# Kernel optimization log

Hardware: AMD Instinct MI355X
Metric: run time of the kernel (lower is better)

## Reference

```python
import jax, jax.numpy as jnp
import numpy as np


def setup_inputs() -> dict:
    key = jax.random.key(0)
    k1, k2 = jax.random.split(key)
    hw, bs, c = 16384, 16, 256
    nq = 100
    return {
        "query_feat": jax.random.normal(k1, (hw, bs, c), dtype=jnp.float32),
        "support_feat": jax.random.normal(k2, (nq, bs, c), dtype=jnp.float32),
        "h": 128,
        "w": 128,
    }


def reference(query_feat, support_feat, h, w):
    # query_feat: [hw, bs, c], support_feat: [nq, bs, c]
    hw, bs, c = query_feat.shape
    nq = support_feat.shape[0]
    dtype = query_feat.dtype

    side_normalizer = jnp.array([w, h], dtype=dtype)[None, None, :]  # [1,1,2]

    q = jnp.transpose(query_feat, (1, 0, 2))    # [bs, hw, c]
    s = jnp.transpose(support_feat, (1, 0, 2))  # [bs, nq, c]

    # bmm(q, s^T) -> [bs, hw, nq]; transpose -> [bs, nq, hw]
    similarity_flat = jnp.einsum('bnc,bkc->bnk', s, q)        # [bs, nq, hw]
    similarity = similarity_flat.reshape(bs, nq, h, w)

    # coordinate grid: stack([grid_x, grid_y]) with 'ij' meshgrid, flattened to [hw, 2]
    ys = jnp.linspace(0.5, h - 0.5, h, dtype=jnp.float32)
    xs = jnp.linspace(0.5, w - 0.5, w, dtype=jnp.float32)
    grid_y, grid_x = jnp.meshgrid(ys, xs, indexing='ij')      # [h, w] each
    coord = jnp.stack([grid_x, grid_y], axis=-1).reshape(hw, 2)  # [hw, 2]

    similarity_softmax = jax.nn.softmax(similarity_flat, axis=-1)  # [bs, nq, hw]

    proposal_for_loss = jnp.einsum('bnk,kd->bnd', similarity_softmax, coord) / side_normalizer

    # peak masking: argmax -> one_hot -> reshape (w, h) [faithful to original swap] -> 3x3 max pool
    max_pos = jnp.argmax(similarity_flat, axis=-1)            # [bs, nq]
    max_mask = jax.nn.one_hot(max_pos, hw, dtype=jnp.float32).reshape(bs, nq, w, h)
    local_max_mask = jax.lax.reduce_window(
        max_mask, -jnp.inf, jax.lax.max,
        window_dimensions=(1, 1, 3, 3), window_strides=(1, 1, 1, 1),
        padding=((0, 0), (0, 0), (1, 1), (1, 1)),
    ).reshape(bs, nq, hw)                                     # [bs, nq, hw]

    local_sm = similarity_softmax * local_max_mask            # [bs, nq, hw]
    local_sm = local_sm / (jnp.sum(local_sm, axis=-1, keepdims=True) + 1e-10)
    proposals = jnp.einsum('bnk,kd->bnd', local_sm, coord) / side_normalizer

    return (proposal_for_loss, similarity, proposals)
```

## Files before the change

### kernel.cpp

```cpp
#include <hip/hip_runtime.h>
#include <math.h>

#define HW   16384
#define BS   16
#define C    256
#define NQ   100
#define NQP  112
#define Hh   128
#define Ww   128

#define SIM_OFF   3200
#define PROPS_OFF (3200 + 26214400)

#define BM 256
#define BK 32

typedef _Float16 half8 __attribute__((ext_vector_type(8)));
typedef float f32x4 __attribute__((ext_vector_type(4)));

__device__ __forceinline__ void gll16(const void* gp, void* lp) {
    __builtin_amdgcn_global_load_lds((const __attribute__((address_space(1))) void*)gp,
                                     (__attribute__((address_space(3))) void*)lp, 16, 0, 0);
}

__device__ __forceinline__ void split8(const float4 a, const float4 b, half8& hi, half8& lo) {
    float f[8] = {a.x, a.y, a.z, a.w, b.x, b.y, b.z, b.w};
    _Float16 h[8], l[8];
    #pragma unroll
    for (int i = 0; i < 8; ++i) {
        h[i] = (_Float16)f[i];
        l[i] = (_Float16)(f[i] - (float)h[i]);
    }
    hi = *(half8*)h;
    lo = *(half8*)l;
}

__global__ __launch_bounds__(256) void split_S_kernel(const float* __restrict__ S,
                                                      _Float16* __restrict__ shi,
                                                      _Float16* __restrict__ slo)
{
    int idx4 = blockIdx.x * 256 + threadIdx.x;
    int idx = idx4 * 4;
    if (idx >= BS * NQP * C) return;
    int b = idx / (NQP * C);
    int rem = idx - b * (NQP * C);
    int n = rem / C;
    int k = rem - n * C;
    float4 v = make_float4(0.f, 0.f, 0.f, 0.f);
    if (n < NQ) v = *(const float4*)(S + ((size_t)n * BS + b) * C + k);
    _Float16 h[4], l[4];
    float f[4] = {v.x, v.y, v.z, v.w};
    #pragma unroll
    for (int i = 0; i < 4; ++i) {
        h[i] = (_Float16)f[i];
        l[i] = (_Float16)(f[i] - (float)h[i]);
    }
    *(uint2*)(shi + idx) = *(uint2*)h;
    *(uint2*)(slo + idx) = *(uint2*)l;
}

template<bool USE_WS>
__global__ __launch_bounds__(256, 2) void gemm_kernel(const float* __restrict__ Q,
                                                      const float* __restrict__ S,
                                                      const _Float16* __restrict__ ShiG,
                                                      const _Float16* __restrict__ SloG,
                                                      float* __restrict__ out)
{
    __shared__ __align__(16) float    Qf[BM * BK];
    __shared__ __align__(16) _Float16 SHI[NQP * BK];
    __shared__ __align__(16) _Float16 SLO[NQP * BK];

    const int b    = blockIdx.y;
    const int hw0  = blockIdx.x * BM;
    const int t    = threadIdx.x;
    const int wid  = t >> 6;
    const int lane = t & 63;
    const int lr   = lane & 15;
    const int lg   = lane >> 4;

    f32x4 acc[7][4];
    #pragma unroll
    for (int n = 0; n < 7; ++n)
        #pragma unroll
        for (int m = 0; m < 4; ++m)
            acc[n][m] = (f32x4)(0.f);

    const int q_r8  = lane >> 3;
    const int q_gc  = (lane & 7) ^ q_r8;
    const int s_r   = lane >> 2;
    const int s_gc  = (lane & 3) ^ ((lane >> 3) & 3);

    for (int k0 = 0; k0 < C; k0 += BK) {
        #pragma unroll
        for (int p = 0; p < 8; ++p) {
            int rt = wid * 64 + p * 8;
            const float* g = Q + ((size_t)(hw0 + rt + q_r8) * BS + b) * C + k0 + q_gc * 4;
            gll16(g, &Qf[rt * BK]);
        }
        if (USE_WS) {
            for (int i = wid; i < 14; i += 4) {
                _Float16* arr = (i < 7) ? SHI : SLO;
                const _Float16* src = (i < 7) ? ShiG : SloG;
                int r0 = (i % 7) * 16;
                const _Float16* g = src + ((size_t)b * NQP + r0 + s_r) * C + k0 + s_gc * 8;
                gll16(g, &arr[r0 * BK]);
            }
        }
        __syncthreads();

        half8 bhi[4], blo[4];
        #pragma unroll
        for (int m = 0; m < 4; ++m) {
            int row = wid * 64 + 16 * m + lr;
            int r7 = row & 7;
            float4 qa = *(const float4*)&Qf[row * BK + (((2 * lg + 0) ^ r7) << 2)];
            float4 qb = *(const float4*)&Qf[row * BK + (((2 * lg + 1) ^ r7) << 2)];
            split8(qa, qb, bhi[m], blo[m]);
        }

        #pragma unroll
        for (int n = 0; n < 7; ++n) {
            int row = 16 * n + lr;
            half8 ahi, alo;
            if (USE_WS) {
                int slot = lg ^ ((row >> 1) & 3);
                ahi = *(const half8*)&SHI[row * BK + slot * 8];
                alo = *(const half8*)&SLO[row * BK + slot * 8];
            } else {
                if (row < NQ) {
                    const float* g = S + ((size_t)row * BS + b) * C + k0 + 8 * lg;
                    float4 sa = *(const float4*)g;
                    float4 sb = *(const float4*)(g + 4);
                    split8(sa, sb, ahi, alo);
                } else {
                    ahi = (half8)(_Float16)0.f;
                    alo = (half8)(_Float16)0.f;
                }
            }
            #pragma unroll
            for (int m = 0; m < 4; ++m) {
                acc[n][m] = __builtin_amdgcn_mfma_f32_16x16x32_f16(ahi, bhi[m], acc[n][m], 0, 0, 0);
                acc[n][m] = __builtin_amdgcn_mfma_f32_16x16x32_f16(ahi, blo[m], acc[n][m], 0, 0, 0);
                acc[n][m] = __builtin_amdgcn_mfma_f32_16x16x32_f16(alo, bhi[m], acc[n][m], 0, 0, 0);
            }
        }
        __syncthreads();
    }

    float* simb = out + SIM_OFF;
    #pragma unroll
    for (int n = 0; n < 7; ++n) {
        #pragma unroll
        for (int j = 0; j < 4; ++j) {
            int row = 16 * n + 4 * lg + j;
            if (row < NQ) {
                size_t base = ((size_t)(b * NQ + row)) * HW + hw0 + wid * 64 + lr;
                #pragma unroll
                for (int m = 0; m < 4; ++m)
                    simb[base + 16 * m] = acc[n][m][j];
            }
        }
    }
}

__global__ __launch_bounds__(256) void reduce_kernel(const float* __restrict__ sim,
                                                     float* __restrict__ out)
{
    __shared__ float rowbuf[HW];
    __shared__ float s_pm[4];
    __shared__ int   s_pi[4];
    __shared__ float s_red[4][3];
    __shared__ float s_gmax;
    __shared__ int   s_gidx;

    const int row = blockIdx.x;
    const int t   = threadIdx.x;
    const int wid  = t >> 6;
    const int lane = t & 63;
    const float4* src4 = (const float4*)(sim + (size_t)row * HW);

    float vmax = -3.4e38f;
    int   vidx = 0;
    #pragma unroll
    for (int p = 0; p < 16; ++p) {
        int i4 = p * 256 + t;
        float4 v = src4[i4];
        *(float4*)&rowbuf[i4 * 4] = v;
        int base = i4 * 4;
        if (v.x > vmax) { vmax = v.x; vidx = base; }
        if (v.y > vmax) { vmax = v.y; vidx = base + 1; }
        if (v.z > vmax) { vmax = v.z; vidx = base + 2; }
        if (v.w > vmax) { vmax = v.w; vidx = base + 3; }
    }
    #pragma unroll
    for (int off = 32; off > 0; off >>= 1) {
        float ov = __shfl_down(vmax, off);
        int   oi = __shfl_down(vidx, off);
        if (ov > vmax || (ov == vmax && oi < vidx)) { vmax = ov; vidx = oi; }
    }
    if (lane == 0) { s_pm[wid] = vmax; s_pi[wid] = vidx; }
    __syncthreads();
    if (t == 0) {
        float gm = s_pm[0]; int gi = s_pi[0];
        #pragma unroll
        for (int wv = 1; wv < 4; ++wv) {
            float ov = s_pm[wv]; int oi = s_pi[wv];
            if (ov > gm || (ov == gm && oi < gi)) { gm = ov; gi = oi; }
        }
        s_gmax = gm; s_gidx = gi;
    }
    __syncthreads();
    const float gmax = s_gmax;

    float z = 0.f, wx = 0.f, wy = 0.f;
    #pragma unroll
    for (int p = 0; p < 16; ++p) {
        int i4 = p * 256 + t;
        float4 v = *(const float4*)&rowbuf[i4 * 4];
        int i = i4 * 4;
        float e0 = __expf(v.x - gmax), e1 = __expf(v.y - gmax);
        float e2 = __expf(v.z - gmax), e3 = __expf(v.w - gmax);
        z += (e0 + e1) + (e2 + e3);
        float cy = (float)(i >> 7) + 0.5f;
        float cx0 = (float)(i & (Ww - 1)) + 0.5f;
        wx += e0 * cx0 + e1 * (cx0 + 1.f) + e2 * (cx0 + 2.f) + e3 * (cx0 + 3.f);
        wy += (e0 + e1 + e2 + e3) * cy;
    }
    #pragma unroll
    for (int off = 32; off > 0; off >>= 1) {
        z  += __shfl_down(z, off);
        wx += __shfl_down(wx, off);
        wy += __shfl_down(wy, off);
    }
    if (lane == 0) { s_red[wid][0] = z; s_red[wid][1] = wx; s_red[wid][2] = wy; }
    __syncthreads();

    if (t == 0) {
        float Z = 0.f, WX = 0.f, WY = 0.f;
        #pragma unroll
        for (int wv = 0; wv < 4; ++wv) { Z += s_red[wv][0]; WX += s_red[wv][1]; WY += s_red[wv][2]; }

        out[(size_t)row * 2 + 0] = (WX / Z) * (1.0f / (float)Ww);
        out[(size_t)row * 2 + 1] = (WY / Z) * (1.0f / (float)Hh);

        int p  = s_gidx;
        int pr = p / Hh;
        int pc = p % Hh;
        float lsum = 0.f, lwx = 0.f, lwy = 0.f;
        #pragma unroll
        for (int di = -1; di <= 1; ++di) {
            #pragma unroll
            for (int dj = -1; dj <= 1; ++dj) {
                int r = pr + di, c = pc + dj;
                if (r >= 0 && r < Ww && c >= 0 && c < Hh) {
                    int k = r * Hh + c;
                    float e = __expf(rowbuf[k] - gmax);
                    lsum += e;
                    lwx  += e * ((float)(k & (Ww - 1)) + 0.5f);
                    lwy  += e * ((float)(k >> 7) + 0.5f);
                }
            }
        }
        float denom = lsum + 1e-10f * Z;
        out[PROPS_OFF + (size_t)row * 2 + 0] = (lwx / denom) * (1.0f / (float)Ww);
        out[PROPS_OFF + (size_t)row * 2 + 1] = (lwy / denom) * (1.0f / (float)Hh);
    }
}

extern "C" void kernel_launch(void* const* d_in, const int* in_sizes, int n_in,
                              void* d_out, int out_size, void* d_ws, size_t ws_size,
                              hipStream_t stream) {
    const float* Q = (const float*)d_in[0];
    const float* S = (const float*)d_in[1];
    float* out = (float*)d_out;

    const size_t splitElems = (size_t)BS * NQP * C;
    const size_t wsNeeded = splitElems * 2 * sizeof(_Float16);

    if (ws_size >= wsNeeded) {
        _Float16* shi = (_Float16*)d_ws;
        _Float16* slo = shi + splitElems;
        split_S_kernel<<<dim3((splitElems / 4 + 255) / 256), 256, 0, stream>>>(S, shi, slo);
        gemm_kernel<true><<<dim3(HW / BM, BS), 256, 0, stream>>>(Q, S, shi, slo, out);
    } else {
        gemm_kernel<false><<<dim3(HW / BM, BS), 256, 0, stream>>>(Q, S, nullptr, nullptr, out);
    }
    reduce_kernel<<<dim3(BS * NQ), 256, 0, stream>>>(out + SIM_OFF, out);
}
```

Baseline: 117.5 us.

## Fuse softmax partial reductions into GEMM epilogue and double-buffer LDS staging

```diff
diff --git a/kernel.cpp b/kernel.cpp
--- a/kernel.cpp
+++ b/kernel.cpp
@@ -12,8 +12,9 @@
 #define SIM_OFF   3200
 #define PROPS_OFF (3200 + 26214400)
 
-#define BM 256
+#define BM 128
 #define BK 32
+#define NBLK (HW / BM)
 
 typedef _Float16 half8 __attribute__((ext_vector_type(8)));
 typedef float f32x4 __attribute__((ext_vector_type(4)));
@@ -64,11 +65,17 @@
                                                       const float* __restrict__ S,
                                                       const _Float16* __restrict__ ShiG,
                                                       const _Float16* __restrict__ SloG,
-                                                      float* __restrict__ out)
+                                                      float* __restrict__ out,
+                                                      float* __restrict__ pm,
+                                                      float* __restrict__ pz,
+                                                      float* __restrict__ pwx,
+                                                      int* __restrict__ pidx)
 {
-    __shared__ __align__(16) float    Qf[BM * BK];
-    __shared__ __align__(16) _Float16 SHI[NQP * BK];
-    __shared__ __align__(16) _Float16 SLO[NQP * BK];
+    __shared__ __align__(16) float    Qf[2][BM * BK];
+    __shared__ __align__(16) _Float16 SHI[2][NQP * BK];
+    __shared__ __align__(16) _Float16 SLO[2][NQP * BK];
+    __shared__ float Lm[NQP][4], Lz[NQP][4], Lwx[NQP][4];
+    __shared__ int   Li[NQP][4];
 
     const int b    = blockIdx.y;
     const int hw0  = blockIdx.x * BM;
@@ -78,54 +85,54 @@
     const int lr   = lane & 15;
     const int lg   = lane >> 4;
 
-    f32x4 acc[7][4];
+    f32x4 acc[7][2];
     #pragma unroll
     for (int n = 0; n < 7; ++n)
         #pragma unroll
-        for (int m = 0; m < 4; ++m)
+        for (int m = 0; m < 2; ++m)
             acc[n][m] = (f32x4)(0.f);
 
-    const int q_r8  = lane >> 3;
-    const int q_gc  = (lane & 7) ^ q_r8;
-    const int s_r   = lane >> 2;
-    const int s_gc  = (lane & 3) ^ ((lane >> 3) & 3);
-
-    for (int k0 = 0; k0 < C; k0 += BK) {
-        #pragma unroll
-        for (int p = 0; p < 8; ++p) {
-            int rt = wid * 64 + p * 8;
+    const int q_r8 = lane >> 3;
+    const int q_gc = (lane & 7) ^ q_r8;
+    const int s_r  = lane >> 2;
+    const int s_gc = (lane & 3) ^ ((lane >> 3) & 3);
+
+    auto stageQ = [&](int buf, int k0) {
+        #pragma unroll
+        for (int p = 0; p < 4; ++p) {
+            int rt = wid * 8 + p * 32;
             const float* g = Q + ((size_t)(hw0 + rt + q_r8) * BS + b) * C + k0 + q_gc * 4;
-            gll16(g, &Qf[rt * BK]);
-        }
-        if (USE_WS) {
-            for (int i = wid; i < 14; i += 4) {
-                _Float16* arr = (i < 7) ? SHI : SLO;
-                const _Float16* src = (i < 7) ? ShiG : SloG;
-                int r0 = (i % 7) * 16;
-                const _Float16* g = src + ((size_t)b * NQP + r0 + s_r) * C + k0 + s_gc * 8;
-                gll16(g, &arr[r0 * BK]);
-            }
-        }
-        __syncthreads();
-
-        half8 bhi[4], blo[4];
-        #pragma unroll
-        for (int m = 0; m < 4; ++m) {
-            int row = wid * 64 + 16 * m + lr;
+            gll16(g, &Qf[buf][rt * BK]);
+        }
+    };
+    auto stageS = [&](int buf, int k0) {
+        for (int i = wid; i < 14; i += 4) {
+            int r0 = (i % 7) * 16;
+            _Float16* dst = (i < 7) ? &SHI[buf][r0 * BK] : &SLO[buf][r0 * BK];
+            const _Float16* src = (i < 7) ? ShiG : SloG;
+            const _Float16* g = src + ((size_t)b * NQP + r0 + s_r) * C + k0 + s_gc * 8;
+            gll16(g, dst);
+        }
+    };
+
+    auto compute = [&](int buf, int k0) {
+        half8 bhi[2], blo[2];
+        #pragma unroll
+        for (int m = 0; m < 2; ++m) {
+            int row = wid * 32 + 16 * m + lr;
             int r7 = row & 7;
-            float4 qa = *(const float4*)&Qf[row * BK + (((2 * lg + 0) ^ r7) << 2)];
-            float4 qb = *(const float4*)&Qf[row * BK + (((2 * lg + 1) ^ r7) << 2)];
+            float4 qa = *(const float4*)&Qf[buf][row * BK + (((2 * lg + 0) ^ r7) << 2)];
+            float4 qb = *(const float4*)&Qf[buf][row * BK + (((2 * lg + 1) ^ r7) << 2)];
             split8(qa, qb, bhi[m], blo[m]);
         }
-
         #pragma unroll
         for (int n = 0; n < 7; ++n) {
             int row = 16 * n + lr;
             half8 ahi, alo;
             if (USE_WS) {
                 int slot = lg ^ ((row >> 1) & 3);
-                ahi = *(const half8*)&SHI[row * BK + slot * 8];
-                alo = *(const half8*)&SLO[row * BK + slot * 8];
+                ahi = *(const half8*)&SHI[buf][row * BK + slot * 8];
+                alo = *(const half8*)&SLO[buf][row * BK + slot * 8];
             } else {
                 if (row < NQ) {
                     const float* g = S + ((size_t)row * BS + b) * C + k0 + 8 * lg;
@@ -138,12 +145,25 @@
                 }
             }
             #pragma unroll
-            for (int m = 0; m < 4; ++m) {
+            for (int m = 0; m < 2; ++m) {
                 acc[n][m] = __builtin_amdgcn_mfma_f32_16x16x32_f16(ahi, bhi[m], acc[n][m], 0, 0, 0);
                 acc[n][m] = __builtin_amdgcn_mfma_f32_16x16x32_f16(ahi, blo[m], acc[n][m], 0, 0, 0);
                 acc[n][m] = __builtin_amdgcn_mfma_f32_16x16x32_f16(alo, bhi[m], acc[n][m], 0, 0, 0);
             }
         }
+    };
+
+    stageQ(0, 0);
+    if (USE_WS) stageS(0, 0);
+    __syncthreads();
+    #pragma unroll
+    for (int step = 0; step < 8; ++step) {
+        int curb = step & 1;
+        if (step < 7) {
+            stageQ(curb ^ 1, (step + 1) * BK);
+            if (USE_WS) stageS(curb ^ 1, (step + 1) * BK);
+        }
+        compute(curb, step * BK);
         __syncthreads();
     }
 
@@ -153,13 +173,114 @@
         #pragma unroll
         for (int j = 0; j < 4; ++j) {
             int row = 16 * n + 4 * lg + j;
+            float v0 = acc[n][0][j], v1 = acc[n][1][j];
+            int col0 = wid * 32 + lr, col1 = col0 + 16;
             if (row < NQ) {
-                size_t base = ((size_t)(b * NQ + row)) * HW + hw0 + wid * 64 + lr;
+                size_t base = ((size_t)(b * NQ + row)) * HW + hw0 + col0;
+                simb[base]      = v0;
+                simb[base + 16] = v1;
+            }
+            if (USE_WS) {
+                float vm; int ci;
+                if (v0 >= v1) { vm = v0; ci = col0; } else { vm = v1; ci = col1; }
                 #pragma unroll
-                for (int m = 0; m < 4; ++m)
-                    simb[base + 16 * m] = acc[n][m][j];
-            }
-        }
+                for (int off = 1; off < 16; off <<= 1) {
+                    float ov = __shfl_xor(vm, off);
+                    int   oc = __shfl_xor(ci, off);
+                    if (ov > vm || (ov == vm && oc < ci)) { vm = ov; ci = oc; }
+                }
+                float e0 = __expf(v0 - vm), e1 = __expf(v1 - vm);
+                float zt = e0 + e1;
+                float wxt = e0 * ((float)col0 + 0.5f) + e1 * ((float)col1 + 0.5f);
+                #pragma unroll
+                for (int off = 1; off < 16; off <<= 1) {
+                    zt  += __shfl_xor(zt, off);
+                    wxt += __shfl_xor(wxt, off);
+                }
+                if (lr == 0) { Lm[row][wid] = vm; Li[row][wid] = ci; Lz[row][wid] = zt; Lwx[row][wid] = wxt; }
+            }
+        }
+    }
+    if (USE_WS) {
+        __syncthreads();
+        if (t < NQ) {
+            int row = t;
+            float M = Lm[row][0]; int gi = Li[row][0];
+            #pragma unroll
+            for (int w = 1; w < 4; ++w) {
+                float ov = Lm[row][w]; int oc = Li[row][w];
+                if (ov > M || (ov == M && oc < gi)) { M = ov; gi = oc; }
+            }
+            float Zp = 0.f, WXp = 0.f;
+            #pragma unroll
+            for (int w = 0; w < 4; ++w) {
+                float s = __expf(Lm[row][w] - M);
+                Zp  += Lz[row][w] * s;
+                WXp += Lwx[row][w] * s;
+            }
+            size_t pbase = ((size_t)(b * NQ + row)) * NBLK + blockIdx.x;
+            pm[pbase] = M; pz[pbase] = Zp; pwx[pbase] = WXp; pidx[pbase] = hw0 + gi;
+        }
+    }
+}
+
+__global__ __launch_bounds__(256) void finalize_kernel(const float* __restrict__ sim,
+                                                       const float* __restrict__ pm,
+                                                       const float* __restrict__ pz,
+                                                       const float* __restrict__ pwx,
+                                                       const int* __restrict__ pidx,
+                                                       float* __restrict__ out)
+{
+    const int row  = blockIdx.x * 4 + (threadIdx.x >> 6);
+    const int lane = threadIdx.x & 63;
+    const size_t base = (size_t)row * NBLK;
+
+    float m0 = pm[base + lane],   m1 = pm[base + lane + 64];
+    float z0 = pz[base + lane],   z1 = pz[base + lane + 64];
+    float x0 = pwx[base + lane],  x1 = pwx[base + lane + 64];
+    int   i0 = pidx[base + lane], i1 = pidx[base + lane + 64];
+
+    float v; int gi;
+    if (m0 > m1 || (m0 == m1 && i0 < i1)) { v = m0; gi = i0; } else { v = m1; gi = i1; }
+    #pragma unroll
+    for (int off = 1; off < 64; off <<= 1) {
+        float ov = __shfl_xor(v, off);
+        int   oi = __shfl_xor(gi, off);
+        if (ov > v || (ov == v && oi < gi)) { v = ov; gi = oi; }
+    }
+    float s0 = __expf(m0 - v), s1 = __expf(m1 - v);
+    float Z  = z0 * s0 + z1 * s1;
+    float WX = x0 * s0 + x1 * s1;
+    float WY = z0 * s0 * ((float)lane + 0.5f) + z1 * s1 * ((float)lane + 64.5f);
+    #pragma unroll
+    for (int off = 1; off < 64; off <<= 1) {
+        Z  += __shfl_xor(Z, off);
+        WX += __shfl_xor(WX, off);
+        WY += __shfl_xor(WY, off);
+    }
+    if (lane == 0) {
+        out[(size_t)row * 2 + 0] = (WX / Z) * (1.f / 128.f);
+        out[(size_t)row * 2 + 1] = (WY / Z) * (1.f / 128.f);
+        const float* srow = sim + (size_t)row * HW;
+        int pr = gi >> 7, pc = gi & 127;
+        float ls = 0.f, lx = 0.f, ly = 0.f;
+        #pragma unroll
+        for (int dr = -1; dr <= 1; ++dr) {
+            #pragma unroll
+            for (int dc = -1; dc <= 1; ++dc) {
+                int r = pr + dr, c = pc + dc;
+                if (r >= 0 && r < Ww && c >= 0 && c < Hh) {
+                    int k = r * Hh + c;
+                    float e = __expf(srow[k] - v);
+                    ls += e;
+                    lx += e * ((float)(k & 127) + 0.5f);
+                    ly += e * ((float)(k >> 7) + 0.5f);
+                }
+            }
+        }
+        float denom = ls + 1e-10f * Z;
+        out[PROPS_OFF + (size_t)row * 2 + 0] = (lx / denom) * (1.f / 128.f);
+        out[PROPS_OFF + (size_t)row * 2 + 1] = (ly / denom) * (1.f / 128.f);
     }
 }
 
@@ -275,15 +396,24 @@
     float* out = (float*)d_out;
 
     const size_t splitElems = (size_t)BS * NQP * C;
-    const size_t wsNeeded = splitElems * 2 * sizeof(_Float16);
+    const size_t splitBytes = splitElems * 2 * sizeof(_Float16);
+    const size_t nPart = (size_t)BS * NQ * NBLK;
+    const size_t pOff  = (splitBytes + 255) & ~(size_t)255;
+    const size_t wsNeeded = pOff + nPart * 4 * sizeof(float);
 
     if (ws_size >= wsNeeded) {
         _Float16* shi = (_Float16*)d_ws;
         _Float16* slo = shi + splitElems;
-        split_S_kernel<<<dim3((splitElems / 4 + 255) / 256), 256, 0, stream>>>(S, shi, slo);
-        gemm_kernel<true><<<dim3(HW / BM, BS), 256, 0, stream>>>(Q, S, shi, slo, out);
+        float* pm  = (float*)((char*)d_ws + pOff);
+        float* pz  = pm + nPart;
+        float* pwx = pz + nPart;
+        int*   pidx = (int*)(pwx + nPart);
+        split_S_kernel<<<dim3((unsigned)((splitElems / 4 + 255) / 256)), 256, 0, stream>>>(S, shi, slo);
+        gemm_kernel<true><<<dim3(HW / BM, BS), 256, 0, stream>>>(Q, S, shi, slo, out, pm, pz, pwx, pidx);
+        finalize_kernel<<<dim3(BS * NQ / 4), 256, 0, stream>>>(out + SIM_OFF, pm, pz, pwx, pidx, out);
     } else {
-        gemm_kernel<false><<<dim3(HW / BM, BS), 256, 0, stream>>>(Q, S, nullptr, nullptr, out);
-    }
-    reduce_kernel<<<dim3(BS * NQ), 256, 0, stream>>>(out + SIM_OFF, out);
-}
+        gemm_kernel<false><<<dim3(HW / BM, BS), 256, 0, stream>>>(Q, S, nullptr, nullptr, out,
+                                                                  nullptr, nullptr, nullptr, nullptr);
+        reduce_kernel<<<dim3(BS * NQ), 256, 0, stream>>>(out + SIM_OFF, out);
+    }
+}
```

New measurement: 164.2 us. +39.8%, slower.
